# Performance work log

Measured on AMD Instinct MI355X. Metric: run time of the kernel, lower is better.

The kernel has to match this reference:

```python
import jax, jax.numpy as jnp
import numpy as np

B, S, D = 4, 4096, 512


def setup_inputs() -> dict:
    key = jax.random.key(0)
    ks = jax.random.split(key, 9)
    sc = 1.0 / np.sqrt(D)
    return {
        "xs": jax.random.normal(ks[0], (B, S, D), dtype=jnp.float32),
        "Wk": jax.random.normal(ks[1], (D, D), dtype=jnp.float32) * sc,
        "bk": jax.random.normal(ks[2], (D,), dtype=jnp.float32) * 0.01,
        "Wq": jax.random.normal(ks[3], (D, D), dtype=jnp.float32) * sc,
        "bq": jax.random.normal(ks[4], (D,), dtype=jnp.float32) * 0.01,
        "Wv": jax.random.normal(ks[5], (D, D), dtype=jnp.float32) * sc,
        "bv": jax.random.normal(ks[6], (D,), dtype=jnp.float32) * 0.01,
        "Wl": jax.random.normal(ks[7], (D, D), dtype=jnp.float32) * sc,
        "bl": jax.random.normal(ks[8], (D,), dtype=jnp.float32) * 0.01,
    }


def reference(xs, Wk, bk, Wq, bq, Wv, bv, Wl, bl):
    dim = xs.shape[-1]
    K = xs @ Wk.T + bk          # [B,S,D]
    Q = xs @ Wq.T + bq          # [B,S,D]
    V = xs @ Wv.T + bv          # [B,S,D]
    # qk[b,s,e] = sum_d K[b,s,d] * Q[b,e,d]  (torch einsum 'bsd,bde->bse' with Q^T)
    qk = jnp.einsum('bsd,bed->bse', K, Q)   # [B,S,S]
    # softmax over dim 1 (the 's' axis), after dividing by dim
    a = jax.nn.softmax(qk / dim, axis=1)    # [B,S,S]
    # torch einsum 'bij,bik->bik': sum over j then broadcast-multiply with V
    rowsum = jnp.sum(a, axis=2)             # [B,S]
    attn = rowsum[:, :, None] * V           # [B,S,D]
    return jnp.tanh(attn @ Wl.T + bl)
```

## Files before the change

kernel.cpp:

```cpp
#include <hip/hip_runtime.h>
#include <cstdint>

#define B_ 4
#define S_ 4096
#define D_ 512
#define M_ (B_*S_)

typedef _Float16 f16;
typedef _Float16 f16x8 __attribute__((ext_vector_type(8)));
typedef _Float16 f16x4 __attribute__((ext_vector_type(4)));
typedef _Float16 f16x2 __attribute__((ext_vector_type(2)));
typedef float    f32x4 __attribute__((ext_vector_type(4)));

typedef __attribute__((address_space(1))) void* as1p;
typedef __attribute__((address_space(3))) void* as3p;

__device__ __forceinline__ void gl2lds16(const void* g, void* l) {
    __builtin_amdgcn_global_load_lds((as1p)g, (as3p)l, 16, 0, 0);
}

union f16pack { f16x8 v8; f16x2 v2[4]; };

__global__ __launch_bounds__(256) void prep_tr_kernel(
    const float* __restrict__ xs,
    const float* __restrict__ Wv, const float* __restrict__ Wk,
    const float* __restrict__ Wq, const float* __restrict__ Wl,
    f16* __restrict__ xs_h, float* __restrict__ xsSum,
    f16* __restrict__ WvT, f16* __restrict__ WkT, f16* __restrict__ WqT,
    f16* __restrict__ WlH)
{
    __shared__ float smem[64*68];
    const int t = threadIdx.x;
    if (blockIdx.x < 256) {
        const int blk = blockIdx.x;
        const int w = t >> 6, l = t & 63;
        const int col = l * 8;
        float acc[8] = {0,0,0,0,0,0,0,0};
        for (int c = 0; c < 16; c++) {
            int row = blk*64 + c*4 + w;
            const float4* p = (const float4*)(xs + (size_t)row*512 + col);
            float4 a = p[0], b = p[1];
            f16x8 o;
            o[0]=(f16)a.x; o[1]=(f16)a.y; o[2]=(f16)a.z; o[3]=(f16)a.w;
            o[4]=(f16)b.x; o[5]=(f16)b.y; o[6]=(f16)b.z; o[7]=(f16)b.w;
            *(f16x8*)(xs_h + (size_t)row*512 + col) = o;
            acc[0]+=a.x; acc[1]+=a.y; acc[2]+=a.z; acc[3]+=a.w;
            acc[4]+=b.x; acc[5]+=b.y; acc[6]+=b.z; acc[7]+=b.w;
        }
        #pragma unroll
        for (int q = 0; q < 8; q++) smem[w*512 + col + q] = acc[q];
        __syncthreads();
        const int b = blk >> 6;
        #pragma unroll
        for (int k = 0; k < 2; k++) {
            int c = t + k*256;
            atomicAdd(&xsSum[b*512 + c], smem[c] + smem[512+c] + smem[1024+c] + smem[1536+c]);
        }
        return;
    }
    const int v = blockIdx.x - 256;
    const int z = v >> 6, tile_id = v & 63;
    const int bx = tile_id & 7, by = tile_id >> 3;
    if (z == 3) {
        const size_t base = (size_t)tile_id*4096 + t*16;
        const float4* s4 = (const float4*)(Wl + base);
        float4 a0 = s4[0], a1 = s4[1], a2 = s4[2], a3 = s4[3];
        f16x8 o0, o1;
        o0[0]=(f16)a0.x; o0[1]=(f16)a0.y; o0[2]=(f16)a0.z; o0[3]=(f16)a0.w;
        o0[4]=(f16)a1.x; o0[5]=(f16)a1.y; o0[6]=(f16)a1.z; o0[7]=(f16)a1.w;
        o1[0]=(f16)a2.x; o1[1]=(f16)a2.y; o1[2]=(f16)a2.z; o1[3]=(f16)a2.w;
        o1[4]=(f16)a3.x; o1[5]=(f16)a3.y; o1[6]=(f16)a3.z; o1[7]=(f16)a3.w;
        *(f16x8*)(WlH + base)     = o0;
        *(f16x8*)(WlH + base + 8) = o1;
        return;
    }
    float (*tile)[68] = (float(*)[68])smem;
    const float* src = (z == 0) ? Wv : ((z == 1) ? Wk : Wq);
    f16* dst = (z == 0) ? WvT : ((z == 1) ? WkT : WqT);
    const int i0 = bx*64, j0 = by*64;
    const int r = t >> 2, cpart = (t & 3)*16;
    {
        const float4* s4 = (const float4*)(src + (size_t)(i0 + r)*512 + j0 + cpart);
        float4 a0 = s4[0], a1 = s4[1], a2 = s4[2], a3 = s4[3];
        *(float4*)&tile[r][cpart]    = a0;
        *(float4*)&tile[r][cpart+4]  = a1;
        *(float4*)&tile[r][cpart+8]  = a2;
        *(float4*)&tile[r][cpart+12] = a3;
    }
    __syncthreads();
    const int c = t >> 2, rpart = (t & 3)*16;
    f16x8 o0, o1;
    #pragma unroll
    for (int q = 0; q < 8; q++) o0[q] = (f16)tile[rpart + q][c];
    #pragma unroll
    for (int q = 0; q < 8; q++) o1[q] = (f16)tile[rpart + 8 + q][c];
    *(f16x8*)(dst + (size_t)(j0 + c)*512 + i0 + rpart)     = o0;
    *(f16x8*)(dst + (size_t)(j0 + c)*512 + i0 + rpart + 8) = o1;
}

__global__ __launch_bounds__(256) void wmm_kernel(
    const f16* __restrict__ WlH, const f16* __restrict__ WvT,
    const f16* __restrict__ WkT, const f16* __restrict__ WqT,
    const float* __restrict__ Wl, const float* __restrict__ bv,
    const float* __restrict__ bk, const float* __restrict__ bq,
    f16* __restrict__ WvlH, float* __restrict__ bvlG,
    float* __restrict__ Mm, float* __restrict__ MT,
    float* __restrict__ t1, float* __restrict__ t2, float* __restrict__ t12)
{
    __shared__ f16 lA[64*32];
    __shared__ f16 lB[64*32];
    const int t = threadIdx.x, z = blockIdx.z;
    const int i0 = blockIdx.x*64, j0 = blockIdx.y*64;
    const int lane = t & 63, wid = t >> 6;
    const int wm = (wid & 1)*32, wn = (wid >> 1)*32;
    const f16* A = (z == 0) ? WlH : ((z == 1) ? WkT : WqT);
    const f16* B = (z == 0) ? WvT : ((z == 1) ? WqT : WkT);
    const int srow = t >> 2, skb = (t & 3) << 4;
    const long aoff = (long)(i0 + srow)*1024 + skb;
    const long boff = (long)(j0 + srow)*1024 + skb;
    const unsigned wbase = (unsigned)wid << 10;
    const bool doT1 = (z == 1) && (blockIdx.x == 0);
    const bool doT2 = (z == 1) && (blockIdx.y == 0);
    const int jj = t >> 2, kq = (t & 3)*8;

    f32x4 acc[2][2] = {};
    float t1a = 0.f, t2a = 0.f;
    const int ael = (wm + (lane & 15))*32 + ((lane >> 4) << 3);
    const int bel = (wn + (lane & 15))*32 + ((lane >> 4) << 3);

    for (int k0 = 0; k0 < 512; k0 += 32) {
        __syncthreads();
        gl2lds16((const char*)A + aoff + k0*2, (char*)lA + wbase);
        gl2lds16((const char*)B + boff + k0*2, (char*)lB + wbase);
        __syncthreads();
        f16x8 af[2], bf[2];
        af[0] = *(const f16x8*)(lA + ael);
        af[1] = *(const f16x8*)(lA + ael + 512);
        bf[0] = *(const f16x8*)(lB + bel);
        bf[1] = *(const f16x8*)(lB + bel + 512);
        #pragma unroll
        for (int i = 0; i < 2; i++)
            #pragma unroll
            for (int j = 0; j < 2; j++)
                acc[i][j] = __builtin_amdgcn_mfma_f32_16x16x32_f16(af[i], bf[j], acc[i][j], 0, 0, 0);
        if (doT1) {
            float4 b0 = *(const float4*)(bk + k0 + kq);
            float4 b1 = *(const float4*)(bk + k0 + kq + 4);
            float bb[8] = {b0.x,b0.y,b0.z,b0.w,b1.x,b1.y,b1.z,b1.w};
            #pragma unroll
            for (int q = 0; q < 8; q++) t1a += (float)lB[jj*32 + kq + q] * bb[q];
        }
        if (doT2) {
            float4 b0 = *(const float4*)(bq + k0 + kq);
            float4 b1 = *(const float4*)(bq + k0 + kq + 4);
            float bb[8] = {b0.x,b0.y,b0.z,b0.w,b1.x,b1.y,b1.z,b1.w};
            #pragma unroll
            for (int q = 0; q < 8; q++) t2a += (float)lA[jj*32 + kq + q] * bb[q];
        }
    }

    const int rb = wm + ((lane >> 4) << 2);
    const int cb = wn + (lane & 15);
    if (z == 0) {
        #pragma unroll
        for (int i = 0; i < 2; i++)
            #pragma unroll
            for (int j = 0; j < 2; j++)
                #pragma unroll
                for (int r = 0; r < 4; r++)
                    WvlH[(size_t)(i0 + rb + i*16 + r)*512 + j0 + cb + j*16] = (f16)acc[i][j][r];
        if (blockIdx.y == 0) {
            int r = t >> 2, part = t & 3;
            const float4* wr = (const float4*)(Wl + (size_t)(i0+r)*512 + part*128);
            const float4* bp = (const float4*)(bv + part*128);
            float s = 0.f;
            #pragma unroll 8
            for (int q = 0; q < 32; q++) {
                float4 wv4 = wr[q], b4 = bp[q];
                s += wv4.x*b4.x + wv4.y*b4.y + wv4.z*b4.z + wv4.w*b4.w;
            }
            s += __shfl_xor(s, 1);
            s += __shfl_xor(s, 2);
            if (part == 0) bvlG[i0 + r] = s;
        }
    } else {
        float* Cout = (z == 1) ? Mm : MT;
        #pragma unroll
        for (int i = 0; i < 2; i++)
            #pragma unroll
            for (int j = 0; j < 2; j++)
                #pragma unroll
                for (int r = 0; r < 4; r++)
                    Cout[(size_t)(i0 + rb + i*16 + r)*512 + j0 + cb + j*16] = acc[i][j][r];
        if (doT1) {
            t1a += __shfl_xor(t1a, 1);
            t1a += __shfl_xor(t1a, 2);
            if ((lane & 3) == 0) t1[j0 + jj] = t1a;
        }
        if (doT2) {
            t2a += __shfl_xor(t2a, 1);
            t2a += __shfl_xor(t2a, 2);
            if ((lane & 3) == 0) t2[i0 + jj] = t2a;
        }
        if (z == 1 && blockIdx.x == 0 && blockIdx.y == 0 && wid == 0) {
            float s = 0.f;
            #pragma unroll
            for (int q = 0; q < 8; q++) s += bk[lane + q*64]*bq[lane + q*64];
            #pragma unroll
            for (int m = 1; m < 64; m <<= 1) s += __shfl_xor(s, m);
            if (lane == 0) *t12 = s;
        }
    }
}

__global__ __launch_bounds__(256) void mva_kernel(const float* __restrict__ W,
    const float* __restrict__ vin, const float* __restrict__ bias2,
    const float* __restrict__ bias3, const float* __restrict__ betaG,
    const float* __restrict__ t12G,
    float* __restrict__ oput, f16* __restrict__ oput_h, float* __restrict__ cG)
{
    const int t = threadIdx.x, w = t >> 6, l = t & 63;
    if (blockIdx.x == 32) {
        const float4* b4 = (const float4*)(bias3 + l*8);
        const float4* v4 = (const float4*)(vin + w*512 + l*8);
        float4 b0 = b4[0], b1 = b4[1], v0 = v4[0], v1 = v4[1];
        float s = b0.x*v0.x + b0.y*v0.y + b0.z*v0.z + b0.w*v0.w
                + b1.x*v1.x + b1.y*v1.y + b1.z*v1.z + b1.w*v1.w;
        #pragma unroll
        for (int m = 1; m < 64; m <<= 1) s += __shfl_xor(s, m);
        if (l == 0) {
            float beta = betaG ? betaG[w] : 4096.0f;
            cG[w] = s + beta * (*t12G);
        }
        return;
    }
    float vb[4][8];
    #pragma unroll
    for (int b = 0; b < 4; b++) {
        float4 p0 = *(const float4*)(vin + b*512 + l*8);
        float4 p1 = *(const float4*)(vin + b*512 + l*8 + 4);
        vb[b][0]=p0.x; vb[b][1]=p0.y; vb[b][2]=p0.z; vb[b][3]=p0.w;
        vb[b][4]=p1.x; vb[b][5]=p1.y; vb[b][6]=p1.z; vb[b][7]=p1.w;
    }
    const int r0 = blockIdx.x*16 + w*4;
    float res[4][4];
    #pragma unroll
    for (int r = 0; r < 4; r++) {
        const float4* wr = (const float4*)(W + (size_t)(r0+r)*512 + l*8);
        float4 a = wr[0], c = wr[1];
        float wv[8] = {a.x,a.y,a.z,a.w,c.x,c.y,c.z,c.w};
        #pragma unroll
        for (int b = 0; b < 4; b++) {
            float s = 0.f;
            #pragma unroll
            for (int q = 0; q < 8; q++) s += wv[q]*vb[b][q];
            res[r][b] = s;
        }
    }
    #pragma unroll
    for (int r = 0; r < 4; r++)
        #pragma unroll
        for (int b = 0; b < 4; b++)
            #pragma unroll
            for (int m = 1; m < 64; m <<= 1) res[r][b] += __shfl_xor(res[r][b], m);
    if (l < 4) {
        const float beta = betaG ? betaG[l] : 4096.0f;
        #pragma unroll
        for (int r = 0; r < 4; r++) {
            float val = res[r][l] + beta*bias2[r0 + r];
            oput[l*512 + r0 + r] = val;
            if (oput_h) oput_h[l*512 + r0 + r] = (f16)val;
        }
    }
}

__global__ __launch_bounds__(256) void z_kernel(const f16* __restrict__ xs_h,
    const float* __restrict__ hG, const float* __restrict__ c1G,
    float* __restrict__ yG, float* __restrict__ S0G)
{
    __shared__ float hs[512];
    __shared__ float yred[4][512];
    __shared__ float s0red[4];
    const int blk = blockIdx.x, t = threadIdx.x;
    const int b = blk >> 6, w = t >> 6, l = t & 63;
    hs[t] = hG[b*512 + t]; hs[t+256] = hG[b*512 + t + 256];
    __syncthreads();
    const float c1 = c1G[b];
    float hx[8];
    #pragma unroll
    for (int q = 0; q < 8; q++) hx[q] = hs[l*8+q];
    float yacc[8] = {0,0,0,0,0,0,0,0};
    float s0acc = 0.f;
    for (int it = 0; it < 16; it++) {
        int row = blk*64 + w*16 + it;
        f16x8 v = *(const f16x8*)(xs_h + (size_t)row*512 + l*8);
        float xf[8];
        #pragma unroll
        for (int q = 0; q < 8; q++) xf[q] = (float)v[q];
        float d = 0.f;
        #pragma unroll
        for (int q = 0; q < 8; q++) d += xf[q]*hx[q];
        #pragma unroll
        for (int m = 1; m < 64; m <<= 1) d += __shfl_xor(d, m);
        float z  = 4096.0f + (d + c1)*(1.0f/512.0f);
        float iv = 1.0f/z;
        s0acc += iv;
        #pragma unroll
        for (int q = 0; q < 8; q++) yacc[q] += iv*xf[q];
    }
    #pragma unroll
    for (int q = 0; q < 8; q++) yred[w][l*8+q] = yacc[q];
    if (l == 0) s0red[w] = s0acc;
    __syncthreads();
    #pragma unroll
    for (int k = 0; k < 2; k++) {
        int c = t + k*256;
        atomicAdd(&yG[b*512 + c], yred[0][c]+yred[1][c]+yred[2][c]+yred[3][c]);
    }
    if (t == 0) atomicAdd(&S0G[b], s0red[0]+s0red[1]+s0red[2]+s0red[3]);
}

__global__ __launch_bounds__(256, 2) void vl_gemm(const f16* __restrict__ A,
    const f16* __restrict__ Bt, const float* __restrict__ bvlG,
    const float* __restrict__ blG, const f16* __restrict__ uH,
    const float* __restrict__ c2G, const float* __restrict__ S0G,
    float* __restrict__ out)
{
    constexpr int K = 512;
    __shared__ f16 lA[128*32];
    __shared__ f16 lB[128*32];
    __shared__ float rsbuf[128];
    const int t = threadIdx.x;
    const int m0 = blockIdx.x*128, n0 = blockIdx.y*128;
    const int lane = t & 63, wid = t >> 6;
    const int wm = (wid & 1) << 6, wn = (wid >> 1) << 6;
    const int srow = t >> 2, skb = (t & 3) << 4;
    const long aoff0 = (long)(m0 + srow)*(K*2) + skb;
    const long aoff1 = aoff0 + 64L*(K*2);
    const long boff0 = (long)(n0 + srow)*(K*2) + skb;
    const long boff1 = boff0 + 64L*(K*2);
    char* ldsA = (char*)lA;
    char* ldsB = (char*)lB;
    const unsigned wbase = (unsigned)wid << 10;
    const char* Ab = (const char*)A;
    const char* Bb = (const char*)Bt;

    const int bat = blockIdx.x >> 5;
    const f16* u = uH + bat*512;
    const int ku = (lane >> 4) << 3;

    f32x4 acc[4][4] = {};
    float racc[4] = {0.f,0.f,0.f,0.f};
    const int ael = (wm + (lane & 15))*32 + ku;
    const int bel = (wn + (lane & 15))*32 + ku;

    for (int k0 = 0; k0 < K; k0 += 32) {
        __syncthreads();
        const long kb = (long)k0*2;
        gl2lds16(Ab + aoff0 + kb, ldsA + wbase);
        gl2lds16(Ab + aoff1 + kb, ldsA + 4096 + wbase);
        gl2lds16(Bb + boff0 + kb, ldsB + wbase);
        gl2lds16(Bb + boff1 + kb, ldsB + 4096 + wbase);
        __syncthreads();
        f16x8 af[4], bf[4];
        #pragma unroll
        for (int i = 0; i < 4; i++) af[i] = *(const f16x8*)(lA + ael + i*512);
        #pragma unroll
        for (int j = 0; j < 4; j++) bf[j] = *(const f16x8*)(lB + bel + j*512);
        f16pack up; up.v8 = *(const f16x8*)(u + k0 + ku);
        #pragma unroll
        for (int i = 0; i < 4; i++) {
            f16pack ap; ap.v8 = af[i];
            #pragma unroll
            for (int q = 0; q < 4; q++)
                racc[i] = __builtin_amdgcn_fdot2(ap.v2[q], up.v2[q], racc[i], false);
        }
        #pragma unroll
        for (int i = 0; i < 4; i++)
            #pragma unroll
            for (int j = 0; j < 4; j++)
                acc[i][j] = __builtin_amdgcn_mfma_f32_16x16x32_f16(af[i], bf[j], acc[i][j], 0, 0, 0);
    }

    #pragma unroll
    for (int i = 0; i < 4; i++) {
        racc[i] += __shfl_xor(racc[i], 16);
        racc[i] += __shfl_xor(racc[i], 32);
    }
    const float S0 = S0G[bat], c2 = c2G[bat];
    if (wid < 2 && lane < 16) {
        #pragma unroll
        for (int i = 0; i < 4; i++)
            rsbuf[wm + i*16 + lane] = S0 + (racc[i] + c2)*(1.0f/512.0f);
    }
    __syncthreads();

    const int crb = m0 + wm + ((lane >> 4) << 2);
    const int ccb = n0 + wn + (lane & 15);
    const int lrb = wm + ((lane >> 4) << 2);
    #pragma unroll
    for (int i = 0; i < 4; i++) {
        float rsv[4];
        #pragma unroll
        for (int r = 0; r < 4; r++) rsv[r] = rsbuf[lrb + i*16 + r];
        #pragma unroll
        for (int j = 0; j < 4; j++) {
            int c = ccb + j*16;
            float bb = bvlG[c], bo = blG[c];
            #pragma unroll
            for (int r = 0; r < 4; r++) {
                float yv = rsv[r]*(acc[i][j][r] + bb) + bo;
                float e2 = __expf(2.0f*yv);
                out[(size_t)(crb + i*16 + r)*512 + c] = 1.0f - 2.0f/(e2 + 1.0f);
            }
        }
    }
}

extern "C" void kernel_launch(void* const* d_in, const int* in_sizes, int n_in,
                              void* d_out, int out_size, void* d_ws, size_t ws_size,
                              hipStream_t stream)
{
    const float* xs = (const float*)d_in[0];
    const float* Wk = (const float*)d_in[1];
    const float* bk = (const float*)d_in[2];
    const float* Wq = (const float*)d_in[3];
    const float* bq = (const float*)d_in[4];
    const float* Wv = (const float*)d_in[5];
    const float* bv = (const float*)d_in[6];
    const float* Wl = (const float*)d_in[7];
    const float* bl = (const float*)d_in[8];
    float* out = (float*)d_out;

    char* w = (char*)d_ws;
    f16*   xs_h = (f16*)w;   w += (size_t)M_*D_*2;
    f16*   WvlH = (f16*)w;   w += (size_t)D_*D_*2;
    f16*   WlH  = (f16*)w;   w += (size_t)D_*D_*2;
    f16*   WvT  = (f16*)w;   w += (size_t)D_*D_*2;
    f16*   WkT  = (f16*)w;   w += (size_t)D_*D_*2;
    f16*   WqT  = (f16*)w;   w += (size_t)D_*D_*2;
    float* Mm   = (float*)w; w += (size_t)D_*D_*4;
    float* MT   = (float*)w; w += (size_t)D_*D_*4;
    float* xsSum= (float*)w; w += (size_t)B_*D_*4;
    float* yG   = (float*)w; w += (size_t)B_*D_*4;
    float* S0G  = (float*)w; w += 4*4;
    f16*   uH   = (f16*)w;   w += (size_t)B_*D_*2;
    float* hG   = (float*)w; w += (size_t)B_*D_*4;
    float* uG   = (float*)w; w += (size_t)B_*D_*4;
    float* t1   = (float*)w; w += (size_t)D_*4;
    float* t2   = (float*)w; w += (size_t)D_*4;
    float* bvlG = (float*)w; w += (size_t)D_*4;
    float* c1G  = (float*)w; w += 4*4;
    float* c2G  = (float*)w; w += 4*4;
    float* t12  = (float*)w; w += 4;
    if ((size_t)(w - (char*)d_ws) > ws_size) return;

    hipMemsetAsync(xsSum, 0, (2*B_*D_ + 4)*sizeof(float), stream);
    prep_tr_kernel<<<512, 256, 0, stream>>>(xs, Wv, Wk, Wq, Wl,
        xs_h, xsSum, WvT, WkT, WqT, WlH);
    wmm_kernel<<<dim3(8,8,3), 256, 0, stream>>>(WlH, WvT, WkT, WqT, Wl, bv, bk, bq,
        WvlH, bvlG, Mm, MT, t1, t2, t12);
    mva_kernel<<<33, 256, 0, stream>>>(MT, xsSum, t1, t2, nullptr, t12, hG, nullptr, c1G);
    z_kernel<<<256, 256, 0, stream>>>(xs_h, hG, c1G, yG, S0G);
    mva_kernel<<<33, 256, 0, stream>>>(Mm, yG, t2, t1, S0G, t12, uG, uH, c2G);
    vl_gemm<<<dim3(128,4), 256, 0, stream>>>(xs_h, WvlH, bvlG, bl, uH, c2G, S0G, out);
}
```

Before: 158.1 us.

## Fuse front-end kernels into one cooperative kernel with grid syncs

Merges the prep, weight-product, two matrix-vector and z-reduction kernels into a single cooperative kernel of 512 blocks separated by grid-wide syncs. The xs conversion work is split into smaller jobs and partly overlapped with the weight GEMM phase, so blocks that would otherwise idle stay busy. The aim is to remove several kernel launch gaps and tail effects. The cost is that grid.sync barriers are not free, and every block must be co-resident, which needs 2 blocks per CU.

```diff
diff --git a/kernel.cpp b/kernel.cpp
--- a/kernel.cpp
+++ b/kernel.cpp
@@ -1,5 +1,8 @@
 #include <hip/hip_runtime.h>
+#include <hip/hip_cooperative_groups.h>
 #include <cstdint>
+
+namespace cg = cooperative_groups;
 
 #define B_ 4
 #define S_ 4096
@@ -8,7 +11,6 @@
 
 typedef _Float16 f16;
 typedef _Float16 f16x8 __attribute__((ext_vector_type(8)));
-typedef _Float16 f16x4 __attribute__((ext_vector_type(4)));
 typedef _Float16 f16x2 __attribute__((ext_vector_type(2)));
 typedef float    f32x4 __attribute__((ext_vector_type(4)));
 
@@ -21,48 +23,16 @@
 
 union f16pack { f16x8 v8; f16x2 v2[4]; };
 
-__global__ __launch_bounds__(256) void prep_tr_kernel(
-    const float* __restrict__ xs,
+__device__ __forceinline__ void weight_job(int v, int t, char* SMEM,
     const float* __restrict__ Wv, const float* __restrict__ Wk,
     const float* __restrict__ Wq, const float* __restrict__ Wl,
-    f16* __restrict__ xs_h, float* __restrict__ xsSum,
     f16* __restrict__ WvT, f16* __restrict__ WkT, f16* __restrict__ WqT,
     f16* __restrict__ WlH)
 {
-    __shared__ float smem[64*68];
-    const int t = threadIdx.x;
-    if (blockIdx.x < 256) {
-        const int blk = blockIdx.x;
-        const int w = t >> 6, l = t & 63;
-        const int col = l * 8;
-        float acc[8] = {0,0,0,0,0,0,0,0};
-        for (int c = 0; c < 16; c++) {
-            int row = blk*64 + c*4 + w;
-            const float4* p = (const float4*)(xs + (size_t)row*512 + col);
-            float4 a = p[0], b = p[1];
-            f16x8 o;
-            o[0]=(f16)a.x; o[1]=(f16)a.y; o[2]=(f16)a.z; o[3]=(f16)a.w;
-            o[4]=(f16)b.x; o[5]=(f16)b.y; o[6]=(f16)b.z; o[7]=(f16)b.w;
-            *(f16x8*)(xs_h + (size_t)row*512 + col) = o;
-            acc[0]+=a.x; acc[1]+=a.y; acc[2]+=a.z; acc[3]+=a.w;
-            acc[4]+=b.x; acc[5]+=b.y; acc[6]+=b.z; acc[7]+=b.w;
-        }
-        #pragma unroll
-        for (int q = 0; q < 8; q++) smem[w*512 + col + q] = acc[q];
-        __syncthreads();
-        const int b = blk >> 6;
-        #pragma unroll
-        for (int k = 0; k < 2; k++) {
-            int c = t + k*256;
-            atomicAdd(&xsSum[b*512 + c], smem[c] + smem[512+c] + smem[1024+c] + smem[1536+c]);
-        }
-        return;
-    }
-    const int v = blockIdx.x - 256;
     const int z = v >> 6, tile_id = v & 63;
     const int bx = tile_id & 7, by = tile_id >> 3;
     if (z == 3) {
-        const size_t base = (size_t)tile_id*4096 + t*16;
+        const size_t base = (size_t)tile_id*4096 + (size_t)t*16;
         const float4* s4 = (const float4*)(Wl + base);
         float4 a0 = s4[0], a1 = s4[1], a2 = s4[2], a3 = s4[3];
         f16x8 o0, o1;
@@ -74,7 +44,7 @@
         *(f16x8*)(WlH + base + 8) = o1;
         return;
     }
-    float (*tile)[68] = (float(*)[68])smem;
+    float (*tile)[68] = (float(*)[68])SMEM;
     const float* src = (z == 0) ? Wv : ((z == 1) ? Wk : Wq);
     f16* dst = (z == 0) ? WvT : ((z == 1) ? WkT : WqT);
     const int i0 = bx*64, j0 = by*64;
@@ -98,7 +68,37 @@
     *(f16x8*)(dst + (size_t)(j0 + c)*512 + i0 + rpart + 8) = o1;
 }
 
-__global__ __launch_bounds__(256) void wmm_kernel(
+__device__ __forceinline__ void xs_job(int j, int t, char* SMEM,
+    const float* __restrict__ xs, f16* __restrict__ xs_h,
+    float* __restrict__ xsSum)
+{
+    float* red = (float*)SMEM;
+    const int w = t >> 6, l = t & 63;
+    const int col = l * 8;
+    float acc[8] = {0,0,0,0,0,0,0,0};
+    for (int c = 0; c < 8; c++) {
+        int row = j*32 + c*4 + w;
+        const float4* p = (const float4*)(xs + (size_t)row*512 + col);
+        float4 a = p[0], b = p[1];
+        f16x8 o;
+        o[0]=(f16)a.x; o[1]=(f16)a.y; o[2]=(f16)a.z; o[3]=(f16)a.w;
+        o[4]=(f16)b.x; o[5]=(f16)b.y; o[6]=(f16)b.z; o[7]=(f16)b.w;
+        *(f16x8*)(xs_h + (size_t)row*512 + col) = o;
+        acc[0]+=a.x; acc[1]+=a.y; acc[2]+=a.z; acc[3]+=a.w;
+        acc[4]+=b.x; acc[5]+=b.y; acc[6]+=b.z; acc[7]+=b.w;
+    }
+    #pragma unroll
+    for (int q = 0; q < 8; q++) red[w*512 + col + q] = acc[q];
+    __syncthreads();
+    const int b = j >> 7;
+    #pragma unroll
+    for (int k = 0; k < 2; k++) {
+        int c = t + k*256;
+        atomicAdd(&xsSum[b*512 + c], red[c] + red[512+c] + red[1024+c] + red[1536+c]);
+    }
+}
+
+__device__ __forceinline__ void wmm_job(int blk, int t, char* SMEM,
     const f16* __restrict__ WlH, const f16* __restrict__ WvT,
     const f16* __restrict__ WkT, const f16* __restrict__ WqT,
     const float* __restrict__ Wl, const float* __restrict__ bv,
@@ -107,10 +107,11 @@
     float* __restrict__ Mm, float* __restrict__ MT,
     float* __restrict__ t1, float* __restrict__ t2, float* __restrict__ t12)
 {
-    __shared__ f16 lA[64*32];
-    __shared__ f16 lB[64*32];
-    const int t = threadIdx.x, z = blockIdx.z;
-    const int i0 = blockIdx.x*64, j0 = blockIdx.y*64;
+    f16* lA = (f16*)SMEM;
+    f16* lB = lA + 64*32;
+    const int z = blk >> 6, rr = blk & 63;
+    const int bx = rr & 7, by = rr >> 3;
+    const int i0 = bx*64, j0 = by*64;
     const int lane = t & 63, wid = t >> 6;
     const int wm = (wid & 1)*32, wn = (wid >> 1)*32;
     const f16* A = (z == 0) ? WlH : ((z == 1) ? WkT : WqT);
@@ -119,8 +120,8 @@
     const long aoff = (long)(i0 + srow)*1024 + skb;
     const long boff = (long)(j0 + srow)*1024 + skb;
     const unsigned wbase = (unsigned)wid << 10;
-    const bool doT1 = (z == 1) && (blockIdx.x == 0);
-    const bool doT2 = (z == 1) && (blockIdx.y == 0);
+    const bool doT1 = (z == 1) && (bx == 0);
+    const bool doT2 = (z == 1) && (by == 0);
     const int jj = t >> 2, kq = (t & 3)*8;
 
     f32x4 acc[2][2] = {};
@@ -169,7 +170,7 @@
                 #pragma unroll
                 for (int r = 0; r < 4; r++)
                     WvlH[(size_t)(i0 + rb + i*16 + r)*512 + j0 + cb + j*16] = (f16)acc[i][j][r];
-        if (blockIdx.y == 0) {
+        if (by == 0) {
             int r = t >> 2, part = t & 3;
             const float4* wr = (const float4*)(Wl + (size_t)(i0+r)*512 + part*128);
             const float4* bp = (const float4*)(bv + part*128);
@@ -202,7 +203,7 @@
             t2a += __shfl_xor(t2a, 2);
             if ((lane & 3) == 0) t2[i0 + jj] = t2a;
         }
-        if (z == 1 && blockIdx.x == 0 && blockIdx.y == 0 && wid == 0) {
+        if (z == 1 && rr == 0 && wid == 0) {
             float s = 0.f;
             #pragma unroll
             for (int q = 0; q < 8; q++) s += bk[lane + q*64]*bq[lane + q*64];
@@ -213,14 +214,14 @@
     }
 }
 
-__global__ __launch_bounds__(256) void mva_kernel(const float* __restrict__ W,
-    const float* __restrict__ vin, const float* __restrict__ bias2,
-    const float* __restrict__ bias3, const float* __restrict__ betaG,
-    const float* __restrict__ t12G,
+__device__ __forceinline__ void mva_job(int blk, int t,
+    const float* __restrict__ W, const float* __restrict__ vin,
+    const float* __restrict__ bias2, const float* __restrict__ bias3,
+    const float* __restrict__ betaG, const float* __restrict__ t12G,
     float* __restrict__ oput, f16* __restrict__ oput_h, float* __restrict__ cG)
 {
-    const int t = threadIdx.x, w = t >> 6, l = t & 63;
-    if (blockIdx.x == 32) {
+    const int w = t >> 6, l = t & 63;
+    if (blk == 32) {
         const float4* b4 = (const float4*)(bias3 + l*8);
         const float4* v4 = (const float4*)(vin + w*512 + l*8);
         float4 b0 = b4[0], b1 = b4[1], v0 = v4[0], v1 = v4[1];
@@ -242,7 +243,7 @@
         vb[b][0]=p0.x; vb[b][1]=p0.y; vb[b][2]=p0.z; vb[b][3]=p0.w;
         vb[b][4]=p1.x; vb[b][5]=p1.y; vb[b][6]=p1.z; vb[b][7]=p1.w;
     }
-    const int r0 = blockIdx.x*16 + w*4;
+    const int r0 = blk*16 + w*4;
     float res[4][4];
     #pragma unroll
     for (int r = 0; r < 4; r++) {
@@ -274,15 +275,14 @@
     }
 }
 
-__global__ __launch_bounds__(256) void z_kernel(const f16* __restrict__ xs_h,
-    const float* __restrict__ hG, const float* __restrict__ c1G,
-    float* __restrict__ yG, float* __restrict__ S0G)
-{
-    __shared__ float hs[512];
-    __shared__ float yred[4][512];
-    __shared__ float s0red[4];
-    const int blk = blockIdx.x, t = threadIdx.x;
-    const int b = blk >> 6, w = t >> 6, l = t & 63;
+__device__ __forceinline__ void z_job(int blk, int t, char* SMEM,
+    const f16* __restrict__ xs_h, const float* __restrict__ hG,
+    const float* __restrict__ c1G, float* __restrict__ yG, float* __restrict__ S0G)
+{
+    float* hs    = (float*)SMEM;
+    float* yred  = hs + 512;
+    float* s0red = yred + 2048;
+    const int b = blk >> 7, w = t >> 6, l = t & 63;
     hs[t] = hG[b*512 + t]; hs[t+256] = hG[b*512 + t + 256];
     __syncthreads();
     const float c1 = c1G[b];
@@ -291,8 +291,8 @@
     for (int q = 0; q < 8; q++) hx[q] = hs[l*8+q];
     float yacc[8] = {0,0,0,0,0,0,0,0};
     float s0acc = 0.f;
-    for (int it = 0; it < 16; it++) {
-        int row = blk*64 + w*16 + it;
+    for (int it = 0; it < 8; it++) {
+        int row = blk*32 + w*8 + it;
         f16x8 v = *(const f16x8*)(xs_h + (size_t)row*512 + l*8);
         float xf[8];
         #pragma unroll
@@ -309,15 +309,54 @@
         for (int q = 0; q < 8; q++) yacc[q] += iv*xf[q];
     }
     #pragma unroll
-    for (int q = 0; q < 8; q++) yred[w][l*8+q] = yacc[q];
+    for (int q = 0; q < 8; q++) yred[w*512 + l*8+q] = yacc[q];
     if (l == 0) s0red[w] = s0acc;
     __syncthreads();
     #pragma unroll
     for (int k = 0; k < 2; k++) {
         int c = t + k*256;
-        atomicAdd(&yG[b*512 + c], yred[0][c]+yred[1][c]+yred[2][c]+yred[3][c]);
+        atomicAdd(&yG[b*512 + c], yred[c]+yred[512+c]+yred[1024+c]+yred[1536+c]);
     }
     if (t == 0) atomicAdd(&S0G[b], s0red[0]+s0red[1]+s0red[2]+s0red[3]);
+}
+
+__global__ __launch_bounds__(256, 2) void front_kernel(
+    const float* __restrict__ xs,
+    const float* __restrict__ Wv, const float* __restrict__ Wk,
+    const float* __restrict__ Wq, const float* __restrict__ Wl,
+    const float* __restrict__ bv, const float* __restrict__ bk,
+    const float* __restrict__ bq,
+    f16* __restrict__ xs_h, float* __restrict__ xsSum,
+    f16* __restrict__ WvT, f16* __restrict__ WkT, f16* __restrict__ WqT,
+    f16* __restrict__ WlH, f16* __restrict__ WvlH, float* __restrict__ bvlG,
+    float* __restrict__ Mm, float* __restrict__ MT,
+    float* __restrict__ t1, float* __restrict__ t2, float* __restrict__ t12,
+    float* __restrict__ hG, float* __restrict__ c1G,
+    float* __restrict__ yG, float* __restrict__ S0G,
+    float* __restrict__ uG, f16* __restrict__ uH, float* __restrict__ c2G)
+{
+    __shared__ __attribute__((aligned(16))) char SMEM[17408];
+    cg::grid_group grid = cg::this_grid();
+    const int blk = blockIdx.x;
+    const int t = threadIdx.x;
+
+    if (blk < 256) weight_job(blk, t, SMEM, Wv, Wk, Wq, Wl, WvT, WkT, WqT, WlH);
+    else           xs_job(blk - 256, t, SMEM, xs, xs_h, xsSum);
+    grid.sync();
+
+    if (blk < 192)      wmm_job(blk, t, SMEM, WlH, WvT, WkT, WqT, Wl, bv, bk, bq,
+                                WvlH, bvlG, Mm, MT, t1, t2, t12);
+    else if (blk < 448) xs_job(blk - 192 + 256, t, SMEM, xs, xs_h, xsSum);
+    grid.sync();
+
+    if (blk < 33) mva_job(blk, t, MT, xsSum, t1, t2, (const float*)nullptr, t12,
+                          hG, (f16*)nullptr, c1G);
+    grid.sync();
+
+    z_job(blk, t, SMEM, xs_h, hG, c1G, yG, S0G);
+    grid.sync();
+
+    if (blk < 33) mva_job(blk, t, Mm, yG, t2, t1, S0G, t12, uG, uH, c2G);
 }
 
 __global__ __launch_bounds__(256, 2) void vl_gemm(const f16* __restrict__ A,
@@ -456,12 +495,18 @@
     if ((size_t)(w - (char*)d_ws) > ws_size) return;
 
     hipMemsetAsync(xsSum, 0, (2*B_*D_ + 4)*sizeof(float), stream);
-    prep_tr_kernel<<<512, 256, 0, stream>>>(xs, Wv, Wk, Wq, Wl,
-        xs_h, xsSum, WvT, WkT, WqT, WlH);
-    wmm_kernel<<<dim3(8,8,3), 256, 0, stream>>>(WlH, WvT, WkT, WqT, Wl, bv, bk, bq,
-        WvlH, bvlG, Mm, MT, t1, t2, t12);
-    mva_kernel<<<33, 256, 0, stream>>>(MT, xsSum, t1, t2, nullptr, t12, hG, nullptr, c1G);
-    z_kernel<<<256, 256, 0, stream>>>(xs_h, hG, c1G, yG, S0G);
-    mva_kernel<<<33, 256, 0, stream>>>(Mm, yG, t2, t1, S0G, t12, uG, uH, c2G);
+
+    void* args[] = {
+        (void*)&xs, (void*)&Wv, (void*)&Wk, (void*)&Wq, (void*)&Wl,
+        (void*)&bv, (void*)&bk, (void*)&bq,
+        (void*)&xs_h, (void*)&xsSum,
+        (void*)&WvT, (void*)&WkT, (void*)&WqT, (void*)&WlH,
+        (void*)&WvlH, (void*)&bvlG, (void*)&Mm, (void*)&MT,
+        (void*)&t1, (void*)&t2, (void*)&t12,
+        (void*)&hG, (void*)&c1G, (void*)&yG, (void*)&S0G,
+        (void*)&uG, (void*)&uH, (void*)&c2G
+    };
+    hipLaunchCooperativeKernel(front_kernel, dim3(512), dim3(256), args, 0, stream);
+
     vl_gemm<<<dim3(128,4), 256, 0, stream>>>(xs_h, WvlH, bvlG, bl, uH, c2G, S0G, out);
 }
```

Measured after the change: 402.3 us. +154.5%, slower.
